# Optimization experiments

Measured on AMD Instinct MI355X. Metric: run time of the kernel, lower is better.

Reference implementation:

```python
import jax, jax.numpy as jnp
from jax import lax
import numpy as np

EPS = 1e-5  # BatchNorm eps (eval mode, fresh running stats: mean=0, var=1)

N, T, H, C = 16, 512, 64, 64
O, K, E = 64, 9, 256


def setup_inputs() -> dict:
    key = jax.random.key(0)
    ks = jax.random.split(key, 16)
    X = jax.random.normal(ks[0], (N, T, H, C), dtype=jnp.float32)
    edges = jax.random.randint(ks[1], (N, 2, E), 0, H, dtype=jnp.int64)
    # att1/att2: Conv2d(C,1,1) == dot over channels + bias
    w_att1 = jax.random.normal(ks[2], (C,), jnp.float32) * (1.0 / np.sqrt(C))
    b_att1 = jax.random.normal(ks[3], (), jnp.float32) * 0.01
    w_att2 = jax.random.normal(ks[4], (C,), jnp.float32) * (1.0 / np.sqrt(C))
    b_att2 = jax.random.normal(ks[5], (), jnp.float32) * 0.01
    # GCN linear
    W_lin = jax.random.normal(ks[6], (O, C), jnp.float32) * (1.0 / np.sqrt(C))
    b_lin = jax.random.normal(ks[7], (O,), jnp.float32) * 0.01
    # tcn: BN -> ReLU -> Conv2d(O,O,(K,1)) -> BN -> Dropout(eval=id)
    bn1_gamma = 1.0 + 0.1 * jax.random.normal(ks[8], (O,), jnp.float32)
    bn1_beta = 0.1 * jax.random.normal(ks[9], (O,), jnp.float32)
    W_tcn = jax.random.normal(ks[10], (O, O, K, 1), jnp.float32) * (1.0 / np.sqrt(O * K))
    b_tcn = jax.random.normal(ks[11], (O,), jnp.float32) * 0.01
    bn2_gamma = 1.0 + 0.1 * jax.random.normal(ks[12], (O,), jnp.float32)
    bn2_beta = 0.1 * jax.random.normal(ks[13], (O,), jnp.float32)
    return dict(X=X, edges=edges, w_att1=w_att1, b_att1=b_att1, w_att2=w_att2,
                b_att2=b_att2, W_lin=W_lin, b_lin=b_lin, bn1_gamma=bn1_gamma,
                bn1_beta=bn1_beta, W_tcn=W_tcn, b_tcn=b_tcn,
                bn2_gamma=bn2_gamma, bn2_beta=bn2_beta)


def _bn_eval(x, gamma, beta):
    # eval-mode BatchNorm2d with running_mean=0, running_var=1; x is (N, Cc, T, H)
    inv = gamma / jnp.sqrt(1.0 + EPS)
    return x * inv[None, :, None, None] + beta[None, :, None, None]


def _forward(X, edges, w_att1, b_att1, w_att2, b_att2, W_lin, b_lin,
             bn1_gamma, bn1_beta, W_tcn, b_tcn, bn2_gamma, bn2_beta):
    n, t, h, c = X.shape
    k = W_tcn.shape[2]
    # --- adjacency from edge lists (duplicates sum, as sparse_coo->to_dense) ---
    bidx = jnp.arange(n)[:, None]
    adj = jnp.zeros((n, h, h), X.dtype).at[bidx, edges[:, 0, :], edges[:, 1, :]].add(1.0)
    # --- attention: a1[n,t,h] + a2[n,t,h'], leaky_relu, softmax over h ---
    a1 = jnp.einsum('nthc,c->nth', X, w_att1) + b_att1
    a2 = jnp.einsum('nthc,c->nth', X, w_att2) + b_att2
    s = jax.nn.leaky_relu(a1[:, :, :, None] + a2[:, :, None, :], 0.01)  # (n,t,h,h')
    att = jax.nn.softmax(s, axis=2)  # softmax over h (dim=1 pre-permute)
    # --- GCN: einsum('nthh,ntho->ntho') only uses diag(adj@att + I) ---
    diag = jnp.einsum('nhk,ntkh->nth', adj, att) + 1.0
    support = jnp.einsum('nthc,oc->ntho', X, W_lin) + b_lin  # (n,t,h,O)
    g = diag[..., None] * support
    # --- tcn: BN -> ReLU -> temporal conv (K,1) -> BN -> Dropout(eval) ---
    y = jnp.transpose(g, (0, 3, 1, 2))  # (n,O,t,h)
    y = jax.nn.relu(_bn_eval(y, bn1_gamma, bn1_beta))
    pad = (k - 1) // 2
    y = lax.conv_general_dilated(y, W_tcn, window_strides=(1, 1),
                                 padding=[(pad, pad), (0, 0)])
    y = y + b_tcn[None, :, None, None]
    y = _bn_eval(y, bn2_gamma, bn2_beta)
    # --- residual (identity: in==out, stride=1) + relu ---
    y = y + jnp.transpose(X, (0, 3, 1, 2))
    return jnp.transpose(jax.nn.relu(y), (0, 2, 3, 1))  # (n,t,h,O)


def reference(X, edges, w_att1, b_att1, w_att2, b_att2, W_lin, b_lin,
              bn1_gamma, bn1_beta, W_tcn, b_tcn, bn2_gamma, bn2_beta):
    return _forward(X, edges, w_att1, b_att1, w_att2, b_att2, W_lin, b_lin,
                    bn1_gamma, bn1_beta, W_tcn, b_tcn, bn2_gamma, bn2_beta)
```

## Files before the change

kernel.cpp:

```cpp
#include <hip/hip_runtime.h>
#include <hip/hip_bf16.h>
#include <stdint.h>

typedef float f32x4 __attribute__((ext_vector_type(4)));
typedef __bf16 bf16x8 __attribute__((ext_vector_type(8)));
typedef unsigned short u16;
typedef unsigned int u32;

__device__ __forceinline__ u16 f2bf(float f) {
    u32 u = __float_as_uint(f);
    u32 r = (u + 0x7fffu + ((u >> 16) & 1u)) >> 16;
    return (u16)r;
}

__global__ __launch_bounds__(256) void k_adj(const int* __restrict__ edges,
                                             float* __restrict__ adj) {
    __shared__ float a[64 * 64];
    const int n = blockIdx.x;
    for (int i = threadIdx.x; i < 4096; i += 256) a[i] = 0.f;
    __syncthreads();
    {
        int r = edges[n * 512 + threadIdx.x];
        int c = edges[n * 512 + 256 + threadIdx.x];
        atomicAdd(&a[r * 64 + c], 1.0f);
    }
    __syncthreads();
    for (int i = threadIdx.x; i < 4096; i += 256) adj[n * 4096 + i] = a[i];
}

__global__ __launch_bounds__(256) void k_pack(const float* __restrict__ Wlin,
                                              const float* __restrict__ Wtcn,
                                              u16* __restrict__ wlin_p,
                                              u16* __restrict__ wtcn_p) {
    int idx = blockIdx.x * 256 + threadIdx.x;
    if (idx < 4096) {
        int jj = idx & 7, l = (idx >> 3) & 63, j = (idx >> 9) & 3, s = idx >> 11;
        int o = j * 16 + (l & 15);
        int c = s * 32 + (l >> 4) * 8 + jj;
        wlin_p[idx] = f2bf(Wlin[o * 64 + c]);
    }
    int i2 = idx - 4096;
    if (i2 >= 0 && i2 < 36864) {
        int jj = i2 & 7, l = (i2 >> 3) & 63, j = (i2 >> 9) & 3, s = (i2 >> 11) & 1, kk = i2 >> 12;
        int o = j * 16 + (l & 15);
        int op = s * 32 + (l >> 4) * 8 + jj;
        wtcn_p[i2] = f2bf(Wtcn[(o * 64 + op) * 9 + kk]);
    }
}

__global__ __launch_bounds__(256) void k_attn(
    const float* __restrict__ X, const float* __restrict__ adj,
    const float* __restrict__ w1g, const float* __restrict__ b1g,
    const float* __restrict__ w2g, const float* __restrict__ b2g,
    float* __restrict__ diag) {
    __shared__ float adjs[64 * 65];
    __shared__ float p1[64 * 17], p2[64 * 17];
    __shared__ float A1[64], A2[64];

    const int tid = threadIdx.x;
    const int n = blockIdx.x >> 9, t = blockIdx.x & 511;
    const float* Xrow = X + (size_t)(n * 512 + t) * 4096;

    {
        const int c4 = tid & 15;
        const int r0 = tid >> 4;
        float4 wv1 = *(const float4*)(w1g + c4 * 4);
        float4 wv2 = *(const float4*)(w2g + c4 * 4);
#pragma unroll
        for (int i = 0; i < 4; i++) {
            int h = r0 + 16 * i;
            float4 xv = *(const float4*)(Xrow + h * 64 + c4 * 4);
            p1[h * 17 + c4] = xv.x * wv1.x + xv.y * wv1.y + xv.z * wv1.z + xv.w * wv1.w;
            p2[h * 17 + c4] = xv.x * wv2.x + xv.y * wv2.y + xv.z * wv2.z + xv.w * wv2.w;
        }
        const float* adjn = adj + n * 4096;
#pragma unroll
        for (int i = 0; i < 16; i++) {
            int idx = tid + 256 * i;
            adjs[(idx >> 6) * 65 + (idx & 63)] = adjn[idx];
        }
    }
    __syncthreads();

    if (tid < 64) {
        float s = 0.f;
#pragma unroll
        for (int i = 0; i < 16; i++) s += p1[tid * 17 + i];
        A1[tid] = s + b1g[0];
    } else if (tid < 128) {
        int h = tid - 64;
        float s = 0.f;
#pragma unroll
        for (int i = 0; i < 16; i++) s += p2[h * 17 + i];
        A2[h] = s + b2g[0];
    }
    __syncthreads();

    {
        int h = tid >> 2, p = tid & 3;
        float a2h = A2[h];
        float num = 0.f, den = 0.f;
#pragma unroll
        for (int i = 0; i < 16; i++) {
            int k = p * 16 + i;
            float sv = A1[k] + a2h;
            sv = sv > 0.f ? sv : 0.01f * sv;
            float e = __expf(sv);
            den += e;
            num += adjs[h * 65 + k] * e;
        }
        p1[h * 17 + p] = num;
        p2[h * 17 + p] = den;
    }
    __syncthreads();
    if (tid < 64) {
        float num = p1[tid * 17 + 0] + p1[tid * 17 + 1] + p1[tid * 17 + 2] + p1[tid * 17 + 3];
        float den = p2[tid * 17 + 0] + p2[tid * 17 + 1] + p2[tid * 17 + 2] + p2[tid * 17 + 3];
        diag[((size_t)(n * 64 + tid)) * 512 + t] = num / den + 1.0f;
    }
}

__global__ __launch_bounds__(256) void k_gcn_tcn(
    const float* __restrict__ X, const float* __restrict__ diag,
    const u16* __restrict__ wlin_p, const float* __restrict__ blin,
    const float* __restrict__ g1, const float* __restrict__ be1,
    const u16* __restrict__ wtcn_p, const float* __restrict__ btcn,
    const float* __restrict__ g2, const float* __restrict__ be2,
    float* __restrict__ out) {
    __shared__ __align__(16) u16 As[144 * 72];
    __shared__ float DGs[144];

    const int tid = threadIdx.x;
    const int bid = blockIdx.x;
    const int n = bid >> 8, h = (bid >> 2) & 63, tb = (bid & 3) * 128;
    const float* Xbase = X + ((size_t)(n * 512) * 64 + h) * 64;

#pragma unroll
    for (int i = 0; i < 9; i++) {
        int idx = tid + 256 * i;
        int r = idx >> 4, c4 = idx & 15;
        int tg = tb - 4 + r;
        float4 xv = make_float4(0.f, 0.f, 0.f, 0.f);
        if (tg >= 0 && tg < 512) xv = *(const float4*)(Xbase + (size_t)tg * 4096 + c4 * 4);
        uint2 pk;
        pk.x = (u32)f2bf(xv.x) | ((u32)f2bf(xv.y) << 16);
        pk.y = (u32)f2bf(xv.z) | ((u32)f2bf(xv.w) << 16);
        *(uint2*)(&As[r * 72 + c4 * 4]) = pk;
    }
    if (tid < 144) {
        int tg = tb - 4 + tid;
        DGs[tid] = (tg >= 0 && tg < 512) ? diag[((size_t)(n * 64 + h)) * 512 + tg] : 0.f;
    }
    __syncthreads();

    const int w = tid >> 6, l = tid & 63;
    const int col = l & 15, q = l >> 4;
    const float rsf = 1.0f / sqrtf(1.0f + 1e-5f);
    const f32x4 zv = {0.f, 0.f, 0.f, 0.f};

    for (int mt = w; mt < 9; mt += 4) {
        f32x4 acc[4] = {zv, zv, zv, zv};
#pragma unroll
        for (int s = 0; s < 2; s++) {
            bf16x8 a = *(const bf16x8*)(&As[(16 * mt + col) * 72 + s * 32 + q * 8]);
#pragma unroll
            for (int j = 0; j < 4; j++) {
                bf16x8 b = *(const bf16x8*)(&wlin_p[((s * 4 + j) * 64 + l) * 8]);
                acc[j] = __builtin_amdgcn_mfma_f32_16x16x32_bf16(a, b, acc[j], 0, 0, 0);
            }
        }
#pragma unroll
        for (int j = 0; j < 4; j++) {
            int o = 16 * j + col;
            float s1 = g1[o] * rsf;
            float bb = be1[o];
            float bl = blin[o];
#pragma unroll
            for (int rr = 0; rr < 4; rr++) {
                int row = 16 * mt + q * 4 + rr;
                int tg = tb - 4 + row;
                float v = (acc[j][rr] + bl) * DGs[row] * s1 + bb;
                v = v > 0.f ? v : 0.f;
                if (tg < 0 || tg >= 512) v = 0.f;
                As[row * 72 + o] = f2bf(v);
            }
        }
    }
    __syncthreads();

    f32x4 acc2[2][4];
#pragma unroll
    for (int mt = 0; mt < 2; mt++)
#pragma unroll
        for (int j = 0; j < 4; j++) acc2[mt][j] = zv;

    for (int kk = 0; kk < 9; kk++) {
#pragma unroll
        for (int s = 0; s < 2; s++) {
            bf16x8 b[4];
#pragma unroll
            for (int j = 0; j < 4; j++)
                b[j] = *(const bf16x8*)(&wtcn_p[(((kk * 2 + s) * 4 + j) * 64 + l) * 8]);
            bf16x8 a[2];
#pragma unroll
            for (int mt = 0; mt < 2; mt++) {
                int row = 32 * w + 16 * mt + col + kk;
                a[mt] = *(const bf16x8*)(&As[row * 72 + s * 32 + q * 8]);
            }
#pragma unroll
            for (int mt = 0; mt < 2; mt++)
#pragma unroll
                for (int j = 0; j < 4; j++)
                    acc2[mt][j] = __builtin_amdgcn_mfma_f32_16x16x32_bf16(a[mt], b[j], acc2[mt][j], 0, 0, 0);
        }
    }

    float s2[4], c2[4];
#pragma unroll
    for (int j = 0; j < 4; j++) {
        int o = 16 * j + col;
        float s = g2[o] * rsf;
        s2[j] = s;
        c2[j] = btcn[o] * s + be2[o];
    }
#pragma unroll
    for (int mt = 0; mt < 2; mt++) {
#pragma unroll
        for (int rr = 0; rr < 4; rr++) {
            int tt = tb + 32 * w + 16 * mt + 4 * q + rr;
#pragma unroll
            for (int j = 0; j < 4; j++) {
                int o = 16 * j + col;
                size_t off = ((size_t)(n * 512 + tt) * 64 + h) * 64 + o;
                float v = acc2[mt][j][rr] * s2[j] + c2[j] + X[off];
                out[off] = v > 0.f ? v : 0.f;
            }
        }
    }
}

extern "C" void kernel_launch(void* const* d_in, const int* in_sizes, int n_in,
                              void* d_out, int out_size, void* d_ws, size_t ws_size,
                              hipStream_t stream) {
    const float* X    = (const float*)d_in[0];
    const int*  edges = (const int*)d_in[1];
    const float* w1   = (const float*)d_in[2];
    const float* b1   = (const float*)d_in[3];
    const float* w2   = (const float*)d_in[4];
    const float* b2   = (const float*)d_in[5];
    const float* Wlin = (const float*)d_in[6];
    const float* blin = (const float*)d_in[7];
    const float* g1   = (const float*)d_in[8];
    const float* be1  = (const float*)d_in[9];
    const float* Wtcn = (const float*)d_in[10];
    const float* btcn = (const float*)d_in[11];
    const float* g2   = (const float*)d_in[12];
    const float* be2  = (const float*)d_in[13];
    float* out = (float*)d_out;

    char* ws = (char*)d_ws;
    float* adj    = (float*)ws;
    u16*   wlin_p = (u16*)(ws + 262144);
    u16*   wtcn_p = (u16*)(ws + 262144 + 8192);
    float* diag   = (float*)(ws + 262144 + 8192 + 73728);

    hipLaunchKernelGGL(k_adj, dim3(16), dim3(256), 0, stream, edges, adj);
    hipLaunchKernelGGL(k_pack, dim3(160), dim3(256), 0, stream, Wlin, Wtcn, wlin_p, wtcn_p);
    hipLaunchKernelGGL(k_attn, dim3(16 * 512), dim3(256), 0, stream,
                       X, adj, w1, b1, w2, b2, diag);
    hipLaunchKernelGGL(k_gcn_tcn, dim3(16 * 64 * 4), dim3(256), 0, stream,
                       X, diag, wlin_p, blin, g1, be1, wtcn_p, btcn, g2, be2, out);
}
```

Before: 320.0 us.

## Fuse adjacency build and weight packing into attention kernel; per-wave X staging

Removes the separate adjacency and weight-pack launches by folding them into the attention kernel. Each attention block rebuilds its batch's adjacency in shared memory via atomics, and extra tail blocks do the bf16 weight packing. The attention kernel now gives one thread per (t,h), handles four timesteps per block and uses wave shuffles instead of shared-memory reductions. In the GCN/TCN kernel each wave loads and converts its own X rows and diag values just before its MFMA tile, dropping the block-wide barrier, and uses native bf16 conversion. The cost is adjacency being rebuilt redundantly in every attention block.

```diff
diff --git a/kernel.cpp b/kernel.cpp
--- a/kernel.cpp
+++ b/kernel.cpp
@@ -4,6 +4,7 @@
 
 typedef float f32x4 __attribute__((ext_vector_type(4)));
 typedef __bf16 bf16x8 __attribute__((ext_vector_type(8)));
+typedef __bf16 bf16x4 __attribute__((ext_vector_type(4)));
 typedef unsigned short u16;
 typedef unsigned int u32;
 
@@ -13,111 +14,78 @@
     return (u16)r;
 }
 
-__global__ __launch_bounds__(256) void k_adj(const int* __restrict__ edges,
-                                             float* __restrict__ adj) {
-    __shared__ float a[64 * 64];
-    const int n = blockIdx.x;
-    for (int i = threadIdx.x; i < 4096; i += 256) a[i] = 0.f;
+#define NB_ATTN 2048
+
+__global__ __launch_bounds__(256) void k_attn(
+    const float* __restrict__ X, const int* __restrict__ edges,
+    const float* __restrict__ w1g, const float* __restrict__ b1g,
+    const float* __restrict__ w2g, const float* __restrict__ b2g,
+    const float* __restrict__ Wlin, const float* __restrict__ Wtcn,
+    u16* __restrict__ wlin_p, u16* __restrict__ wtcn_p,
+    float* __restrict__ diag) {
+    const int tid = threadIdx.x;
+    const int bid = blockIdx.x;
+
+    if (bid >= NB_ATTN) {
+        int idx = (bid - NB_ATTN) * 256 + tid;
+        if (idx < 4096) {
+            int jj = idx & 7, l = (idx >> 3) & 63, j = (idx >> 9) & 3, s = idx >> 11;
+            int o = j * 16 + (l & 15);
+            int c = s * 32 + (l >> 4) * 8 + jj;
+            wlin_p[idx] = f2bf(Wlin[o * 64 + c]);
+        }
+        int i2 = idx - 4096;
+        if (i2 >= 0 && i2 < 36864) {
+            int jj = i2 & 7, l = (i2 >> 3) & 63, j = (i2 >> 9) & 3, s = (i2 >> 11) & 1, kk = i2 >> 12;
+            int o = j * 16 + (l & 15);
+            int op = s * 32 + (l >> 4) * 8 + jj;
+            wtcn_p[i2] = f2bf(Wtcn[(o * 64 + op) * 9 + kk]);
+        }
+        return;
+    }
+
+    __shared__ __align__(16) float adjs[64 * 65];
+    __shared__ float wl[128];
+
+    const int n = bid >> 7;
+    const int t = (bid & 127) * 4 + (tid >> 6);
+    const int h = tid & 63;
+
+    {
+        f32x4 z4 = {0.f, 0.f, 0.f, 0.f};
+        for (int i = tid; i < 1040; i += 256) *(f32x4*)(&adjs[i * 4]) = z4;
+    }
+    if (tid < 128) wl[tid] = (tid < 64) ? w1g[tid] : w2g[tid - 64];
     __syncthreads();
     {
-        int r = edges[n * 512 + threadIdx.x];
-        int c = edges[n * 512 + 256 + threadIdx.x];
-        atomicAdd(&a[r * 64 + c], 1.0f);
+        int r = edges[n * 512 + tid];
+        int c = edges[n * 512 + 256 + tid];
+        atomicAdd(&adjs[r * 65 + c], 1.0f);
     }
     __syncthreads();
-    for (int i = threadIdx.x; i < 4096; i += 256) adj[n * 4096 + i] = a[i];
-}
-
-__global__ __launch_bounds__(256) void k_pack(const float* __restrict__ Wlin,
-                                              const float* __restrict__ Wtcn,
-                                              u16* __restrict__ wlin_p,
-                                              u16* __restrict__ wtcn_p) {
-    int idx = blockIdx.x * 256 + threadIdx.x;
-    if (idx < 4096) {
-        int jj = idx & 7, l = (idx >> 3) & 63, j = (idx >> 9) & 3, s = idx >> 11;
-        int o = j * 16 + (l & 15);
-        int c = s * 32 + (l >> 4) * 8 + jj;
-        wlin_p[idx] = f2bf(Wlin[o * 64 + c]);
-    }
-    int i2 = idx - 4096;
-    if (i2 >= 0 && i2 < 36864) {
-        int jj = i2 & 7, l = (i2 >> 3) & 63, j = (i2 >> 9) & 3, s = (i2 >> 11) & 1, kk = i2 >> 12;
-        int o = j * 16 + (l & 15);
-        int op = s * 32 + (l >> 4) * 8 + jj;
-        wtcn_p[i2] = f2bf(Wtcn[(o * 64 + op) * 9 + kk]);
-    }
-}
-
-__global__ __launch_bounds__(256) void k_attn(
-    const float* __restrict__ X, const float* __restrict__ adj,
-    const float* __restrict__ w1g, const float* __restrict__ b1g,
-    const float* __restrict__ w2g, const float* __restrict__ b2g,
-    float* __restrict__ diag) {
-    __shared__ float adjs[64 * 65];
-    __shared__ float p1[64 * 17], p2[64 * 17];
-    __shared__ float A1[64], A2[64];
-
-    const int tid = threadIdx.x;
-    const int n = blockIdx.x >> 9, t = blockIdx.x & 511;
-    const float* Xrow = X + (size_t)(n * 512 + t) * 4096;
-
-    {
-        const int c4 = tid & 15;
-        const int r0 = tid >> 4;
-        float4 wv1 = *(const float4*)(w1g + c4 * 4);
-        float4 wv2 = *(const float4*)(w2g + c4 * 4);
-#pragma unroll
-        for (int i = 0; i < 4; i++) {
-            int h = r0 + 16 * i;
-            float4 xv = *(const float4*)(Xrow + h * 64 + c4 * 4);
-            p1[h * 17 + c4] = xv.x * wv1.x + xv.y * wv1.y + xv.z * wv1.z + xv.w * wv1.w;
-            p2[h * 17 + c4] = xv.x * wv2.x + xv.y * wv2.y + xv.z * wv2.z + xv.w * wv2.w;
-        }
-        const float* adjn = adj + n * 4096;
-#pragma unroll
-        for (int i = 0; i < 16; i++) {
-            int idx = tid + 256 * i;
-            adjs[(idx >> 6) * 65 + (idx & 63)] = adjn[idx];
-        }
-    }
-    __syncthreads();
-
-    if (tid < 64) {
-        float s = 0.f;
-#pragma unroll
-        for (int i = 0; i < 16; i++) s += p1[tid * 17 + i];
-        A1[tid] = s + b1g[0];
-    } else if (tid < 128) {
-        int h = tid - 64;
-        float s = 0.f;
-#pragma unroll
-        for (int i = 0; i < 16; i++) s += p2[h * 17 + i];
-        A2[h] = s + b2g[0];
-    }
-    __syncthreads();
-
-    {
-        int h = tid >> 2, p = tid & 3;
-        float a2h = A2[h];
-        float num = 0.f, den = 0.f;
-#pragma unroll
-        for (int i = 0; i < 16; i++) {
-            int k = p * 16 + i;
-            float sv = A1[k] + a2h;
-            sv = sv > 0.f ? sv : 0.01f * sv;
-            float e = __expf(sv);
-            den += e;
-            num += adjs[h * 65 + k] * e;
-        }
-        p1[h * 17 + p] = num;
-        p2[h * 17 + p] = den;
-    }
-    __syncthreads();
-    if (tid < 64) {
-        float num = p1[tid * 17 + 0] + p1[tid * 17 + 1] + p1[tid * 17 + 2] + p1[tid * 17 + 3];
-        float den = p2[tid * 17 + 0] + p2[tid * 17 + 1] + p2[tid * 17 + 2] + p2[tid * 17 + 3];
-        diag[((size_t)(n * 64 + tid)) * 512 + t] = num / den + 1.0f;
-    }
+
+    const float* Xr = X + ((size_t)(n * 512 + t) * 64 + h) * 64;
+    float a1 = b1g[0], a2 = b2g[0];
+#pragma unroll 4
+    for (int c4 = 0; c4 < 16; c4++) {
+        float4 xv = *(const float4*)(Xr + c4 * 4);
+        float4 w1v = *(const float4*)(&wl[c4 * 4]);
+        float4 w2v = *(const float4*)(&wl[64 + c4 * 4]);
+        a1 += xv.x * w1v.x + xv.y * w1v.y + xv.z * w1v.z + xv.w * w1v.w;
+        a2 += xv.x * w2v.x + xv.y * w2v.y + xv.z * w2v.z + xv.w * w2v.w;
+    }
+
+    float num = 0.f, den = 0.f;
+    const float* arow = &adjs[h * 65];
+#pragma unroll
+    for (int k = 0; k < 64; k++) {
+        float s = __shfl(a1, k) + a2;
+        s = fmaxf(s, 0.01f * s);
+        float e = __expf(s);
+        den += e;
+        num = fmaf(arow[k], e, num);
+    }
+    diag[((size_t)(n * 64 + h)) * 512 + t] = num / den + 1.0f;
 }
 
 __global__ __launch_bounds__(256) void k_gcn_tcn(
@@ -128,30 +96,12 @@
     const float* __restrict__ g2, const float* __restrict__ be2,
     float* __restrict__ out) {
     __shared__ __align__(16) u16 As[144 * 72];
-    __shared__ float DGs[144];
 
     const int tid = threadIdx.x;
     const int bid = blockIdx.x;
     const int n = bid >> 8, h = (bid >> 2) & 63, tb = (bid & 3) * 128;
     const float* Xbase = X + ((size_t)(n * 512) * 64 + h) * 64;
-
-#pragma unroll
-    for (int i = 0; i < 9; i++) {
-        int idx = tid + 256 * i;
-        int r = idx >> 4, c4 = idx & 15;
-        int tg = tb - 4 + r;
-        float4 xv = make_float4(0.f, 0.f, 0.f, 0.f);
-        if (tg >= 0 && tg < 512) xv = *(const float4*)(Xbase + (size_t)tg * 4096 + c4 * 4);
-        uint2 pk;
-        pk.x = (u32)f2bf(xv.x) | ((u32)f2bf(xv.y) << 16);
-        pk.y = (u32)f2bf(xv.z) | ((u32)f2bf(xv.w) << 16);
-        *(uint2*)(&As[r * 72 + c4 * 4]) = pk;
-    }
-    if (tid < 144) {
-        int tg = tb - 4 + tid;
-        DGs[tid] = (tg >= 0 && tg < 512) ? diag[((size_t)(n * 64 + h)) * 512 + tg] : 0.f;
-    }
-    __syncthreads();
+    const float* diagb = diag + ((size_t)(n * 64 + h)) * 512;
 
     const int w = tid >> 6, l = tid & 63;
     const int col = l & 15, q = l >> 4;
@@ -159,6 +109,24 @@
     const f32x4 zv = {0.f, 0.f, 0.f, 0.f};
 
     for (int mt = w; mt < 9; mt += 4) {
+#pragma unroll
+        for (int i = 0; i < 4; i++) {
+            int idx = l + 64 * i;
+            int r = 16 * mt + (idx >> 4), c4 = idx & 15;
+            int tg = tb - 4 + r;
+            float4 xv = make_float4(0.f, 0.f, 0.f, 0.f);
+            if (tg >= 0 && tg < 512) xv = *(const float4*)(Xbase + (size_t)tg * 4096 + c4 * 4);
+            bf16x4 pk;
+            pk[0] = (__bf16)xv.x; pk[1] = (__bf16)xv.y;
+            pk[2] = (__bf16)xv.z; pk[3] = (__bf16)xv.w;
+            *(bf16x4*)(&As[r * 72 + c4 * 4]) = pk;
+        }
+        float dg[4];
+#pragma unroll
+        for (int rr = 0; rr < 4; rr++) {
+            int tg = tb - 4 + 16 * mt + q * 4 + rr;
+            dg[rr] = (tg >= 0 && tg < 512) ? diagb[tg] : 0.f;
+        }
         f32x4 acc[4] = {zv, zv, zv, zv};
 #pragma unroll
         for (int s = 0; s < 2; s++) {
@@ -179,10 +147,11 @@
             for (int rr = 0; rr < 4; rr++) {
                 int row = 16 * mt + q * 4 + rr;
                 int tg = tb - 4 + row;
-                float v = (acc[j][rr] + bl) * DGs[row] * s1 + bb;
+                float v = (acc[j][rr] + bl) * dg[rr] * s1 + bb;
                 v = v > 0.f ? v : 0.f;
                 if (tg < 0 || tg >= 512) v = 0.f;
-                As[row * 72 + o] = f2bf(v);
+                __bf16 bv = (__bf16)v;
+                As[row * 72 + o] = __builtin_bit_cast(u16, bv);
             }
         }
     }
@@ -259,15 +228,12 @@
     float* out = (float*)d_out;
 
     char* ws = (char*)d_ws;
-    float* adj    = (float*)ws;
-    u16*   wlin_p = (u16*)(ws + 262144);
-    u16*   wtcn_p = (u16*)(ws + 262144 + 8192);
-    float* diag   = (float*)(ws + 262144 + 8192 + 73728);
-
-    hipLaunchKernelGGL(k_adj, dim3(16), dim3(256), 0, stream, edges, adj);
-    hipLaunchKernelGGL(k_pack, dim3(160), dim3(256), 0, stream, Wlin, Wtcn, wlin_p, wtcn_p);
-    hipLaunchKernelGGL(k_attn, dim3(16 * 512), dim3(256), 0, stream,
-                       X, adj, w1, b1, w2, b2, diag);
+    u16*   wlin_p = (u16*)ws;
+    u16*   wtcn_p = (u16*)(ws + 8192);
+    float* diag   = (float*)(ws + 8192 + 73728);
+
+    hipLaunchKernelGGL(k_attn, dim3(NB_ATTN + 160), dim3(256), 0, stream,
+                       X, edges, w1, b1, w2, b2, Wlin, Wtcn, wlin_p, wtcn_p, diag);
     hipLaunchKernelGGL(k_gcn_tcn, dim3(16 * 64 * 4), dim3(256), 0, stream,
                        X, diag, wlin_p, blin, g1, be1, wtcn_p, btcn, g2, be2, out);
 }
```

Measured after the change: 335.3 us. 4.8% more time.
